# Kernel tuning notes

Measured on AMD Instinct MI355X. Metric: run time of the kernel, lower is better.

The kernel has to match this reference:

```python
import jax, jax.numpy as jnp
import numpy as np

KERNEL_SIZE = 5
EPS = 1e-4


def _sliding_sum(a, k, axis):
    cs = jnp.cumsum(a, axis=axis)
    zshape = list(a.shape)
    zshape[axis] = 1
    cs = jnp.concatenate([jnp.zeros(zshape, a.dtype), cs], axis=axis)
    n = cs.shape[axis]
    hi = jax.lax.slice_in_dim(cs, k, n, axis=axis)
    lo = jax.lax.slice_in_dim(cs, 0, n - k, axis=axis)
    return hi - lo


def box_blur(x, k):
    # x: [B, C, H, W]; normalized box filter with reflect padding (matches kornia box_blur)
    p = k // 2
    xp = jnp.pad(x, ((0, 0), (0, 0), (p, p), (p, p)), mode='reflect')
    s = _sliding_sum(_sliding_sum(xp, k, 2), k, 3)
    return s / jnp.asarray(k * k, x.dtype)


def guided_blur_multichannel(guidance, inp, k, eps):
    B, C, H, W = guidance.shape
    Cp = inp.shape[1]

    mean_I = box_blur(guidance, k)                                   # [B,C,H,W]
    corr_I = box_blur((guidance[:, None] * guidance[:, :, None]).reshape(B, C * C, H, W), k)
    var_I = corr_I.reshape(B, C, C, H, W) - mean_I[:, None] * mean_I[:, :, None]

    mean_p = box_blur(inp, k)                                        # [B,Cp,H,W]
    corr_Ip = box_blur((inp[:, None] * guidance[:, :, None]).reshape(B, C * Cp, H, W), k)
    cov_Ip = corr_Ip.reshape(B, C, Cp, H, W) - mean_p[:, None] * mean_I[:, :, None]

    eye = jnp.eye(C, dtype=guidance.dtype).reshape(1, C, C, 1, 1) * eps
    A = jnp.transpose(var_I + eye, (0, 3, 4, 1, 2))                  # [B,H,W,C,C]
    rhs = jnp.transpose(cov_Ip, (0, 3, 4, 1, 2))                     # [B,H,W,C,Cp]
    a = jnp.linalg.solve(A, rhs)                                     # [B,H,W,C,Cp]

    mean_I_hw = jnp.transpose(mean_I, (0, 2, 3, 1))                  # [B,H,W,C]
    mean_p_hw = jnp.transpose(mean_p, (0, 2, 3, 1))                  # [B,H,W,Cp]
    b = mean_p_hw - jnp.einsum('bhwcp,bhwc->bhwp', a, mean_I_hw)     # [B,H,W,Cp]

    a_ch = jnp.transpose(a.reshape(B, H, W, C * Cp), (0, 3, 1, 2))   # [B,C*Cp,H,W]
    b_ch = jnp.transpose(b, (0, 3, 1, 2))                            # [B,Cp,H,W]
    mean_a = jnp.transpose(box_blur(a_ch, k), (0, 2, 3, 1)).reshape(B, H, W, C, Cp)
    mean_b = box_blur(b_ch, k)                                       # [B,Cp,H,W]

    g_hw = jnp.transpose(guidance, (0, 2, 3, 1))                     # [B,H,W,C]
    out_hw = jnp.einsum('bhwc,bhwcp->bhwp', g_hw, mean_a)            # [B,H,W,Cp]
    return jnp.transpose(out_hw, (0, 3, 1, 2)) + mean_b              # [B,Cp,H,W]


def setup_inputs() -> dict:
    key = jax.random.key(0)
    k1, k2 = jax.random.split(key)
    guidance = jax.random.uniform(k1, (8, 3, 512, 512), dtype=jnp.float32)
    inp = jax.random.uniform(k2, (8, 3, 512, 512), dtype=jnp.float32)
    return {"guidance": guidance, "input": inp}


def reference(guidance, input):
    return guided_blur_multichannel(guidance, input, KERNEL_SIZE, EPS)
```

## Files before the change

### kernel.cpp

```cpp
#include <hip/hip_runtime.h>


namespace {

constexpr int BN = 8;
constexpr int HH = 512;
constexpr int WW = 512;
constexpr int CSZ = HH * WW;
constexpr float GEPS = 1e-4f;
constexpr int SEGW = 8;
constexpr int OUTW = 4 * SEGW;
constexpr int SR   = 16;

__device__ __forceinline__ int refl(int i, int n) {
    if (i < 0) i = -i;
    if (i >= n) i = 2 * n - 2 - i;
    return i;
}

template <int N>
__device__ __forceinline__ float shlN(float v) {
    return __builtin_bit_cast(float,
        __builtin_amdgcn_update_dpp(0, __builtin_bit_cast(int, v),
                                    0x100 + N, 0xF, 0xF, true));
}
__device__ __forceinline__ float hsum5(float v) {
    float t = v + shlN<1>(v);
    float q = t + shlN<2>(t);
    return q + shlN<4>(v);
}

struct St {
    float V1[21];
    float r1[5][6];
    float V2[12];
    float r2[5][12];
};

struct Ctx {
    const float *g0, *g1, *g2, *p0, *p1, *p2;
    float *o0, *o1, *o2;
    int yb, xr, xs;
    bool wr;
};

template <int I, bool SUB1, bool SOLVE, bool V2SUB, bool OUT>
__device__ __forceinline__ void row(St& st, const Ctx& cx, int t) {
    const int rr = 5 * t + I;
    const int y = refl(cx.yb - 4 + rr, HH);
    const int off = y * WW + cx.xr;
    float c0 = cx.g0[off], c1 = cx.g1[off], c2 = cx.g2[off];
    float c3 = cx.p0[off], c4 = cx.p1[off], c5 = cx.p2[off];

    float go0 = 0.f, go1 = 0.f, go2 = 0.f;
    int oOff = 0;
    if constexpr (OUT) {
        oOff = (cx.yb + rr - 8) * WW + cx.xs;
        go0 = cx.g0[oOff]; go1 = cx.g1[oOff]; go2 = cx.g2[oOff];
    }

    st.V1[0] += c0; st.V1[1] += c1; st.V1[2] += c2;
    st.V1[3] += c3; st.V1[4] += c4; st.V1[5] += c5;
    st.V1[6]  += c0 * c0; st.V1[7]  += c0 * c1; st.V1[8]  += c0 * c2;
    st.V1[9]  += c1 * c1; st.V1[10] += c1 * c2; st.V1[11] += c2 * c2;
    st.V1[12] += c0 * c3; st.V1[13] += c0 * c4; st.V1[14] += c0 * c5;
    st.V1[15] += c1 * c3; st.V1[16] += c1 * c4; st.V1[17] += c1 * c5;
    st.V1[18] += c2 * c3; st.V1[19] += c2 * c4; st.V1[20] += c2 * c5;

    if constexpr (SUB1) {
        float o0 = st.r1[I][0], o1 = st.r1[I][1], o2 = st.r1[I][2];
        float o3 = st.r1[I][3], o4 = st.r1[I][4], o5 = st.r1[I][5];
        st.V1[0] -= o0; st.V1[1] -= o1; st.V1[2] -= o2;
        st.V1[3] -= o3; st.V1[4] -= o4; st.V1[5] -= o5;
        st.V1[6]  -= o0 * o0; st.V1[7]  -= o0 * o1; st.V1[8]  -= o0 * o2;
        st.V1[9]  -= o1 * o1; st.V1[10] -= o1 * o2; st.V1[11] -= o2 * o2;
        st.V1[12] -= o0 * o3; st.V1[13] -= o0 * o4; st.V1[14] -= o0 * o5;
        st.V1[15] -= o1 * o3; st.V1[16] -= o1 * o4; st.V1[17] -= o1 * o5;
        st.V1[18] -= o2 * o3; st.V1[19] -= o2 * o4; st.V1[20] -= o2 * o5;
    }
    st.r1[I][0] = c0; st.r1[I][1] = c1; st.r1[I][2] = c2;
    st.r1[I][3] = c3; st.r1[I][4] = c4; st.r1[I][5] = c5;

    if constexpr (SOLVE) {
        float S[21];
#pragma unroll
        for (int c = 0; c < 21; ++c) S[c] = hsum5(st.V1[c]);

        const float nrm = 0.04f;
        float mI0 = S[0] * nrm, mI1 = S[1] * nrm, mI2 = S[2] * nrm;
        float mP0 = S[3] * nrm, mP1 = S[4] * nrm, mP2 = S[5] * nrm;
        float v00 = S[6]  * nrm - mI0 * mI0 + GEPS;
        float v01 = S[7]  * nrm - mI0 * mI1;
        float v02 = S[8]  * nrm - mI0 * mI2;
        float v11 = S[9]  * nrm - mI1 * mI1 + GEPS;
        float v12 = S[10] * nrm - mI1 * mI2;
        float v22 = S[11] * nrm - mI2 * mI2 + GEPS;
        float c00 = S[12] * nrm - mI0 * mP0;
        float c01 = S[13] * nrm - mI0 * mP1;
        float c02 = S[14] * nrm - mI0 * mP2;
        float c10 = S[15] * nrm - mI1 * mP0;
        float c11 = S[16] * nrm - mI1 * mP1;
        float c12 = S[17] * nrm - mI1 * mP2;
        float c20 = S[18] * nrm - mI2 * mP0;
        float c21 = S[19] * nrm - mI2 * mP1;
        float c22 = S[20] * nrm - mI2 * mP2;
        float i00 = v11 * v22 - v12 * v12;
        float i01 = v02 * v12 - v01 * v22;
        float i02 = v01 * v12 - v02 * v11;
        float i11 = v00 * v22 - v02 * v02;
        float i12 = v01 * v02 - v00 * v12;
        float i22 = v00 * v11 - v01 * v01;
        float det = v00 * i00 + v01 * i01 + v02 * i02;
        float rd  = __builtin_amdgcn_rcpf(det);
        float a00 = (i00 * c00 + i01 * c10 + i02 * c20) * rd;
        float a01 = (i00 * c01 + i01 * c11 + i02 * c21) * rd;
        float a02 = (i00 * c02 + i01 * c12 + i02 * c22) * rd;
        float a10 = (i01 * c00 + i11 * c10 + i12 * c20) * rd;
        float a11 = (i01 * c01 + i11 * c11 + i12 * c21) * rd;
        float a12 = (i01 * c02 + i11 * c12 + i12 * c22) * rd;
        float a20 = (i02 * c00 + i12 * c10 + i22 * c20) * rd;
        float a21 = (i02 * c01 + i12 * c11 + i22 * c21) * rd;
        float a22 = (i02 * c02 + i12 * c12 + i22 * c22) * rd;
        float b0 = mP0 - (a00 * mI0 + a10 * mI1 + a20 * mI2);
        float b1 = mP1 - (a01 * mI0 + a11 * mI1 + a21 * mI2);
        float b2 = mP2 - (a02 * mI0 + a12 * mI1 + a22 * mI2);

        float hv[12];
        hv[0] = hsum5(a00); hv[1]  = hsum5(a01); hv[2]  = hsum5(a02);
        hv[3] = hsum5(a10); hv[4]  = hsum5(a11); hv[5]  = hsum5(a12);
        hv[6] = hsum5(a20); hv[7]  = hsum5(a21); hv[8]  = hsum5(a22);
        hv[9] = hsum5(b0);  hv[10] = hsum5(b1);  hv[11] = hsum5(b2);

#pragma unroll
        for (int c = 0; c < 12; ++c) {
            st.V2[c] += hv[c];
            if constexpr (V2SUB) st.V2[c] -= st.r2[I][c];
            st.r2[I][c] = hv[c];
        }

        if constexpr (OUT) {
            float M[12];
#pragma unroll
            for (int c = 0; c < 12; ++c) M[c] = st.V2[c] * 0.04f;
            float o0 = go0 * M[0] + go1 * M[3] + go2 * M[6] + M[9];
            float o1 = go0 * M[1] + go1 * M[4] + go2 * M[7] + M[10];
            float o2 = go0 * M[2] + go1 * M[5] + go2 * M[8] + M[11];
            if (cx.wr) {
                cx.o0[oOff] = o0;
                cx.o1[oOff] = o1;
                cx.o2[oOff] = o2;
            }
        }
    }
}

__global__ __launch_bounds__(64, 2) void fused_kernel(
        const float* __restrict__ g, const float* __restrict__ p,
        float* __restrict__ out) {
    const int lane = threadIdx.x;
    const int l    = lane & 15;
    const int seg  = lane >> 4;
    const int XO   = blockIdx.x * OUTW;
    const int bb   = blockIdx.z;

    const int xbase = XO + seg * SEGW - 2;
    const int xrq   = xbase + l - 2;
    const int xo    = xbase + l + 2;

    Ctx cx;
    cx.g0 = g + (size_t)bb * 3 * CSZ; cx.g1 = cx.g0 + CSZ; cx.g2 = cx.g0 + 2 * CSZ;
    cx.p0 = p + (size_t)bb * 3 * CSZ; cx.p1 = cx.p0 + CSZ; cx.p2 = cx.p0 + 2 * CSZ;
    cx.o0 = out + (size_t)bb * 3 * CSZ; cx.o1 = cx.o0 + CSZ; cx.o2 = cx.o0 + 2 * CSZ;
    cx.yb = blockIdx.y * SR;
    cx.xr = refl(xrq, WW);
    cx.xs = (xo < WW) ? xo : (WW - 1);
    cx.wr = (l < SEGW);

    St st;
#pragma unroll
    for (int i = 0; i < 21; ++i) st.V1[i] = 0.f;
#pragma unroll
    for (int i = 0; i < 12; ++i) st.V2[i] = 0.f;

    row<0, false, false, false, false>(st, cx, 0);
    row<1, false, false, false, false>(st, cx, 0);
    row<2, false, false, false, false>(st, cx, 0);
    row<3, false, false, false, false>(st, cx, 0);
    row<4, false, true,  false, false>(st, cx, 0);
    row<0, true, true, false, false>(st, cx, 1);
    row<1, true, true, false, false>(st, cx, 1);
    row<2, true, true, false, false>(st, cx, 1);
    row<3, true, true, false, true >(st, cx, 1);
    row<4, true, true, true,  true >(st, cx, 1);
#pragma unroll 1
    for (int t = 2; t <= 3; ++t) {
        row<0, true, true, true, true>(st, cx, t);
        row<1, true, true, true, true>(st, cx, t);
        row<2, true, true, true, true>(st, cx, t);
        row<3, true, true, true, true>(st, cx, t);
        row<4, true, true, true, true>(st, cx, t);
    }
    row<0, true, true, true, true>(st, cx, 4);
    row<1, true, true, true, true>(st, cx, 4);
    row<2, true, true, true, true>(st, cx, 4);
    row<3, true, true, true, true>(st, cx, 4);
}

}

extern "C" void kernel_launch(void* const* d_in, const int* in_sizes, int n_in,
                              void* d_out, int out_size, void* d_ws, size_t ws_size,
                              hipStream_t stream) {
    const float* g  = (const float*)d_in[0];
    const float* p  = (const float*)d_in[1];
    float* out = (float*)d_out;

    dim3 grid(WW / OUTW, HH / SR, BN);
    dim3 block(64);

    hipLaunchKernelGGL(fused_kernel, grid, block, 0, stream, g, p, out);
}
```

Measured before the change: 141.8 us.

## Double row strip height and software-prefetch next input row into registers

```diff
diff --git a/kernel.cpp b/kernel.cpp
--- a/kernel.cpp
+++ b/kernel.cpp
@@ -10,7 +10,8 @@
 constexpr float GEPS = 1e-4f;
 constexpr int SEGW = 8;
 constexpr int OUTW = 4 * SEGW;
-constexpr int SR   = 16;
+constexpr int SR   = 32;
+constexpr int NTRIP = (SR + 8) / 5;
 
 __device__ __forceinline__ int refl(int i, int n) {
     if (i < 0) i = -i;
@@ -31,6 +32,7 @@
 }
 
 struct St {
+    float P[6];
     float V1[21];
     float r1[5][6];
     float V2[12];
@@ -44,13 +46,19 @@
     bool wr;
 };
 
-template <int I, bool SUB1, bool SOLVE, bool V2SUB, bool OUT>
+template <int I, bool SUB1, bool SOLVE, bool V2SUB, bool OUT, bool PF>
 __device__ __forceinline__ void row(St& st, const Ctx& cx, int t) {
     const int rr = 5 * t + I;
-    const int y = refl(cx.yb - 4 + rr, HH);
-    const int off = y * WW + cx.xr;
-    float c0 = cx.g0[off], c1 = cx.g1[off], c2 = cx.g2[off];
-    float c3 = cx.p0[off], c4 = cx.p1[off], c5 = cx.p2[off];
+
+    float c0 = st.P[0], c1 = st.P[1], c2 = st.P[2];
+    float c3 = st.P[3], c4 = st.P[4], c5 = st.P[5];
+
+    if constexpr (PF) {
+        const int yn = refl(cx.yb - 4 + rr + 1, HH);
+        const int offn = yn * WW + cx.xr;
+        st.P[0] = cx.g0[offn]; st.P[1] = cx.g1[offn]; st.P[2] = cx.g2[offn];
+        st.P[3] = cx.p0[offn]; st.P[4] = cx.p1[offn]; st.P[5] = cx.p2[offn];
+    }
 
     float go0 = 0.f, go1 = 0.f, go2 = 0.f;
     int oOff = 0;
@@ -182,28 +190,36 @@
 #pragma unroll
     for (int i = 0; i < 12; ++i) st.V2[i] = 0.f;
 
-    row<0, false, false, false, false>(st, cx, 0);
-    row<1, false, false, false, false>(st, cx, 0);
-    row<2, false, false, false, false>(st, cx, 0);
-    row<3, false, false, false, false>(st, cx, 0);
-    row<4, false, true,  false, false>(st, cx, 0);
-    row<0, true, true, false, false>(st, cx, 1);
-    row<1, true, true, false, false>(st, cx, 1);
-    row<2, true, true, false, false>(st, cx, 1);
-    row<3, true, true, false, true >(st, cx, 1);
-    row<4, true, true, true,  true >(st, cx, 1);
+    {
+        const int y0 = refl(cx.yb - 4, HH);
+        const int off0 = y0 * WW + cx.xr;
+        st.P[0] = cx.g0[off0]; st.P[1] = cx.g1[off0]; st.P[2] = cx.g2[off0];
+        st.P[3] = cx.p0[off0]; st.P[4] = cx.p1[off0]; st.P[5] = cx.p2[off0];
+    }
+
+    row<0, false, false, false, false, true>(st, cx, 0);
+    row<1, false, false, false, false, true>(st, cx, 0);
+    row<2, false, false, false, false, true>(st, cx, 0);
+    row<3, false, false, false, false, true>(st, cx, 0);
+    row<4, false, true,  false, false, true>(st, cx, 0);
+    row<0, true, true, false, false, true>(st, cx, 1);
+    row<1, true, true, false, false, true>(st, cx, 1);
+    row<2, true, true, false, false, true>(st, cx, 1);
+    row<3, true, true, false, true,  true>(st, cx, 1);
+    row<4, true, true, true,  true,  true>(st, cx, 1);
 #pragma unroll 1
-    for (int t = 2; t <= 3; ++t) {
-        row<0, true, true, true, true>(st, cx, t);
-        row<1, true, true, true, true>(st, cx, t);
-        row<2, true, true, true, true>(st, cx, t);
-        row<3, true, true, true, true>(st, cx, t);
-        row<4, true, true, true, true>(st, cx, t);
-    }
-    row<0, true, true, true, true>(st, cx, 4);
-    row<1, true, true, true, true>(st, cx, 4);
-    row<2, true, true, true, true>(st, cx, 4);
-    row<3, true, true, true, true>(st, cx, 4);
+    for (int t = 2; t <= 6; ++t) {
+        row<0, true, true, true, true, true>(st, cx, t);
+        row<1, true, true, true, true, true>(st, cx, t);
+        row<2, true, true, true, true, true>(st, cx, t);
+        row<3, true, true, true, true, true>(st, cx, t);
+        row<4, true, true, true, true, true>(st, cx, t);
+    }
+    row<0, true, true, true, true, true >(st, cx, 7);
+    row<1, true, true, true, true, true >(st, cx, 7);
+    row<2, true, true, true, true, true >(st, cx, 7);
+    row<3, true, true, true, true, true >(st, cx, 7);
+    row<4, true, true, true, true, false>(st, cx, 7);
 }
 
 }
```

After: 134.5 us. 1.05x faster.
